# Kernel tuning notes

Hardware: AMD Instinct MI355X
Metric: run time of the kernel (lower is better)

The kernel has to match this reference:

```python
import jax, jax.numpy as jnp
import numpy as np

NQUBIT = 26
WIRES = [0, 1]      # target wires (nt = 2, gate matrix is 4x4)
CONTROLS = [2]      # control wires (nc = 1)


def setup_inputs() -> dict:
    key = jax.random.key(0)
    k1, k2 = jax.random.split(key)
    x = jax.random.normal(k1, (1, 2 ** NQUBIT), dtype=jnp.float32)
    matrix = jax.random.normal(k2, (2 ** len(WIRES), 2 ** len(WIRES)), dtype=jnp.float32)
    return {"x": x, "matrix": matrix}


def reference(x, matrix):
    nt = len(WIRES)
    nc = len(CONTROLS)
    # tensor_rep: [batch] + [2]*nqubit
    x = x.reshape([-1] + [2] * NQUBIT)
    wires = [i + 1 for i in WIRES]
    controls = [i + 1 for i in CONTROLS]
    rest = [p for p in range(NQUBIT + 1) if p not in wires and p not in controls]
    pm_shape = wires + rest + controls
    inv_pm = list(np.argsort(pm_shape))
    # permute targets to front, controls to back, flatten middle
    s = jnp.transpose(x, pm_shape).reshape(2 ** nt, -1, 2 ** nc)  # [4, B*2^23, 2]
    # apply the small gate only on the all-controls-on slice (last index)
    s = s.at[:, :, -1].set(matrix @ s[:, :, -1])
    s = s.reshape([2] * nt + [-1] + [2] * (NQUBIT - nt - nc) + [2] * nc)
    x = jnp.transpose(s, inv_pm)
    # vector_rep + squeeze(0) for batch == 1
    return x.reshape(2 ** NQUBIT, 1)
```

## Files before the change

kernel.cpp:

```cpp
#include <hip/hip_runtime.h>


constexpr unsigned kOff1 = 1u << 24;
constexpr unsigned kOff2 = 1u << 25;
constexpr unsigned kCtrl = 1u << 23;

__global__ __launch_bounds__(256) void gate_kernel(const float* __restrict__ x,
                                                   const float* __restrict__ mat,
                                                   float* __restrict__ out) {
    const unsigned tid = blockIdx.x * blockDim.x + threadIdx.x;
    const unsigned e = tid << 2;

    const float4* __restrict__ x4 = (const float4*)x;
    float4* __restrict__ o4 = (float4*)out;

    const unsigned i0 = e >> 2;
    const unsigned i1 = (e + kOff1) >> 2;
    const unsigned i2 = (e + kOff2) >> 2;
    const unsigned i3 = (e + kOff1 + kOff2) >> 2;

    float4 a0 = x4[i0];
    float4 a1 = x4[i1];
    float4 a2 = x4[i2];
    float4 a3 = x4[i3];

    if (e & kCtrl) {
        float m[16];
#pragma unroll
        for (int k = 0; k < 16; ++k) m[k] = mat[k];

        float4 b0, b1, b2, b3;
        b0.x = m[0]*a0.x + m[1]*a1.x + m[2]*a2.x + m[3]*a3.x;
        b0.y = m[0]*a0.y + m[1]*a1.y + m[2]*a2.y + m[3]*a3.y;
        b0.z = m[0]*a0.z + m[1]*a1.z + m[2]*a2.z + m[3]*a3.z;
        b0.w = m[0]*a0.w + m[1]*a1.w + m[2]*a2.w + m[3]*a3.w;

        b1.x = m[4]*a0.x + m[5]*a1.x + m[6]*a2.x + m[7]*a3.x;
        b1.y = m[4]*a0.y + m[5]*a1.y + m[6]*a2.y + m[7]*a3.y;
        b1.z = m[4]*a0.z + m[5]*a1.z + m[6]*a2.z + m[7]*a3.z;
        b1.w = m[4]*a0.w + m[5]*a1.w + m[6]*a2.w + m[7]*a3.w;

        b2.x = m[8]*a0.x + m[9]*a1.x + m[10]*a2.x + m[11]*a3.x;
        b2.y = m[8]*a0.y + m[9]*a1.y + m[10]*a2.y + m[11]*a3.y;
        b2.z = m[8]*a0.z + m[9]*a1.z + m[10]*a2.z + m[11]*a3.z;
        b2.w = m[8]*a0.w + m[9]*a1.w + m[10]*a2.w + m[11]*a3.w;

        b3.x = m[12]*a0.x + m[13]*a1.x + m[14]*a2.x + m[15]*a3.x;
        b3.y = m[12]*a0.y + m[13]*a1.y + m[14]*a2.y + m[15]*a3.y;
        b3.z = m[12]*a0.z + m[13]*a1.z + m[14]*a2.z + m[15]*a3.z;
        b3.w = m[12]*a0.w + m[13]*a1.w + m[14]*a2.w + m[15]*a3.w;

        a0 = b0; a1 = b1; a2 = b2; a3 = b3;
    }

    o4[i0] = a0;
    o4[i1] = a1;
    o4[i2] = a2;
    o4[i3] = a3;
}

extern "C" void kernel_launch(void* const* d_in, const int* in_sizes, int n_in,
                              void* d_out, int out_size, void* d_ws, size_t ws_size,
                              hipStream_t stream) {
    const float* x   = (const float*)d_in[0];
    const float* mat = (const float*)d_in[1];
    float* out = (float*)d_out;

    const unsigned n_threads = 1u << 22;
    const unsigned block = 256;
    const unsigned grid = n_threads / block;
    gate_kernel<<<grid, block, 0, stream>>>(x, mat, out);
}
```

Before: 447.4 us.

## Split grid into gate blocks and contiguous copy blocks with nontemporal accesses

The grid is split so that half of the blocks apply the 4x4 gate only on the control-on slice. The other half stream-copy the control-off half with contiguous float4 accesses. All loads and stores use nontemporal builtins to avoid polluting the cache. This removes the per-thread control branch and lets copy blocks issue simpler contiguous traffic, at the cost of hardcoded index arithmetic tied to this qubit layout.

```diff
diff --git a/kernel.cpp b/kernel.cpp
--- a/kernel.cpp
+++ b/kernel.cpp
@@ -1,73 +1,67 @@
 #include <hip/hip_runtime.h>
 
 
-constexpr unsigned kOff1 = 1u << 24;
-constexpr unsigned kOff2 = 1u << 25;
-constexpr unsigned kCtrl = 1u << 23;
+typedef float f4 __attribute__((ext_vector_type(4)));
 
-__global__ __launch_bounds__(256) void gate_kernel(const float* __restrict__ x,
+constexpr unsigned kGateBlocks = 8192u;
+constexpr unsigned kQ2f4  = 1u << 21;
+constexpr unsigned kQ1f4  = 1u << 22;
+constexpr unsigned kQ0f4  = 1u << 23;
+
+__global__ __launch_bounds__(256) void gate_kernel(const f4* __restrict__ x4,
                                                    const float* __restrict__ mat,
-                                                   float* __restrict__ out) {
-    const unsigned tid = blockIdx.x * blockDim.x + threadIdx.x;
-    const unsigned e = tid << 2;
+                                                   f4* __restrict__ o4) {
+    const unsigned bid = blockIdx.x;
 
-    const float4* __restrict__ x4 = (const float4*)x;
-    float4* __restrict__ o4 = (float4*)out;
+    if (bid < kGateBlocks) {
+        const unsigned g  = bid * 256u + threadIdx.x;
+        const unsigned i0 = kQ2f4 | g;
+        const unsigned i1 = i0 + kQ1f4;
+        const unsigned i2 = i0 + kQ0f4;
+        const unsigned i3 = i0 + kQ0f4 + kQ1f4;
 
-    const unsigned i0 = e >> 2;
-    const unsigned i1 = (e + kOff1) >> 2;
-    const unsigned i2 = (e + kOff2) >> 2;
-    const unsigned i3 = (e + kOff1 + kOff2) >> 2;
+        const f4 a0 = __builtin_nontemporal_load(&x4[i0]);
+        const f4 a1 = __builtin_nontemporal_load(&x4[i1]);
+        const f4 a2 = __builtin_nontemporal_load(&x4[i2]);
+        const f4 a3 = __builtin_nontemporal_load(&x4[i3]);
 
-    float4 a0 = x4[i0];
-    float4 a1 = x4[i1];
-    float4 a2 = x4[i2];
-    float4 a3 = x4[i3];
-
-    if (e & kCtrl) {
         float m[16];
 #pragma unroll
         for (int k = 0; k < 16; ++k) m[k] = mat[k];
 
-        float4 b0, b1, b2, b3;
-        b0.x = m[0]*a0.x + m[1]*a1.x + m[2]*a2.x + m[3]*a3.x;
-        b0.y = m[0]*a0.y + m[1]*a1.y + m[2]*a2.y + m[3]*a3.y;
-        b0.z = m[0]*a0.z + m[1]*a1.z + m[2]*a2.z + m[3]*a3.z;
-        b0.w = m[0]*a0.w + m[1]*a1.w + m[2]*a2.w + m[3]*a3.w;
+        f4 b0, b1, b2, b3;
+#pragma unroll
+        for (int c = 0; c < 4; ++c) {
+            b0[c] = m[0]*a0[c]  + m[1]*a1[c]  + m[2]*a2[c]  + m[3]*a3[c];
+            b1[c] = m[4]*a0[c]  + m[5]*a1[c]  + m[6]*a2[c]  + m[7]*a3[c];
+            b2[c] = m[8]*a0[c]  + m[9]*a1[c]  + m[10]*a2[c] + m[11]*a3[c];
+            b3[c] = m[12]*a0[c] + m[13]*a1[c] + m[14]*a2[c] + m[15]*a3[c];
+        }
 
-        b1.x = m[4]*a0.x + m[5]*a1.x + m[6]*a2.x + m[7]*a3.x;
-        b1.y = m[4]*a0.y + m[5]*a1.y + m[6]*a2.y + m[7]*a3.y;
-        b1.z = m[4]*a0.z + m[5]*a1.z + m[6]*a2.z + m[7]*a3.z;
-        b1.w = m[4]*a0.w + m[5]*a1.w + m[6]*a2.w + m[7]*a3.w;
-
-        b2.x = m[8]*a0.x + m[9]*a1.x + m[10]*a2.x + m[11]*a3.x;
-        b2.y = m[8]*a0.y + m[9]*a1.y + m[10]*a2.y + m[11]*a3.y;
-        b2.z = m[8]*a0.z + m[9]*a1.z + m[10]*a2.z + m[11]*a3.z;
-        b2.w = m[8]*a0.w + m[9]*a1.w + m[10]*a2.w + m[11]*a3.w;
-
-        b3.x = m[12]*a0.x + m[13]*a1.x + m[14]*a2.x + m[15]*a3.x;
-        b3.y = m[12]*a0.y + m[13]*a1.y + m[14]*a2.y + m[15]*a3.y;
-        b3.z = m[12]*a0.z + m[13]*a1.z + m[14]*a2.z + m[15]*a3.z;
-        b3.w = m[12]*a0.w + m[13]*a1.w + m[14]*a2.w + m[15]*a3.w;
-
-        a0 = b0; a1 = b1; a2 = b2; a3 = b3;
+        __builtin_nontemporal_store(b0, &o4[i0]);
+        __builtin_nontemporal_store(b1, &o4[i1]);
+        __builtin_nontemporal_store(b2, &o4[i2]);
+        __builtin_nontemporal_store(b3, &o4[i3]);
+    } else {
+        const unsigned cb   = bid - kGateBlocks;
+        const unsigned base = cb * 1024u + threadIdx.x;
+#pragma unroll
+        for (int k = 0; k < 4; ++k) {
+            const unsigned t = base + k * 256u;
+            const unsigned s = ((t >> 21) << 22) | (t & 0x1FFFFFu);
+            __builtin_nontemporal_store(__builtin_nontemporal_load(&x4[s]), &o4[s]);
+        }
     }
-
-    o4[i0] = a0;
-    o4[i1] = a1;
-    o4[i2] = a2;
-    o4[i3] = a3;
 }
 
 extern "C" void kernel_launch(void* const* d_in, const int* in_sizes, int n_in,
                               void* d_out, int out_size, void* d_ws, size_t ws_size,
                               hipStream_t stream) {
-    const float* x   = (const float*)d_in[0];
+    const f4* x4  = (const f4*)d_in[0];
     const float* mat = (const float*)d_in[1];
-    float* out = (float*)d_out;
+    f4* o4 = (f4*)d_out;
 
-    const unsigned n_threads = 1u << 22;
+    const unsigned grid  = 16384;
     const unsigned block = 256;
-    const unsigned grid = n_threads / block;
-    gate_kernel<<<grid, block, 0, stream>>>(x, mat, out);
+    gate_kernel<<<grid, block, 0, stream>>>(x4, mat, o4);
 }
```

Result: faster. 423.9 us (-5.3%).
